# Optimization experiments

Measured on AMD Instinct MI355X. Metric: run time of the kernel, lower is better.

Reference implementation:

```python
import jax, jax.numpy as jnp
import numpy as np

D_IN = 768
D_SAE = 768 * 16  # expansion_factor = 16
K = 64
BATCH = 8192


def setup_inputs() -> dict:
    key = jax.random.key(0)
    k1, k2, k3 = jax.random.split(key, 3)
    x = jax.random.normal(k1, (BATCH, D_IN), dtype=jnp.float32)
    # Kaiming-uniform-ish encoder init (exact init values don't matter for correctness)
    bound = (6.0 / D_IN) ** 0.5
    W_enc = jax.random.uniform(k2, (D_IN, D_SAE), dtype=jnp.float32, minval=-bound, maxval=bound)
    b_enc = jnp.zeros((D_SAE,), dtype=jnp.float32)
    W_dec = jax.random.normal(k3, (D_SAE, D_IN), dtype=jnp.float32) * (1.0 / D_IN ** 0.5)
    # unit-norm decoder rows (per the module's normalize_decoder_weights)
    W_dec = W_dec / (jnp.linalg.norm(W_dec, axis=1, keepdims=True) + 1e-8)
    b_dec = jnp.zeros((D_IN,), dtype=jnp.float32)
    return {"x": x, "W_enc": W_enc, "b_enc": b_enc, "W_dec": W_dec, "b_dec": b_dec}


def reference(x, W_enc, b_enc, W_dec, b_dec):
    # encode: center, dense matmul, ReLU
    pre_acts = jax.nn.relu((x - b_dec) @ W_enc + b_enc)  # [B, d_sae]
    # top-k selection per row, scatter back into dense sparse_acts
    topk_vals, topk_idx = jax.lax.top_k(pre_acts, K)  # [B, K]
    rows = jnp.arange(pre_acts.shape[0])[:, None]  # [B, 1]
    sparse_acts = jnp.zeros_like(pre_acts).at[rows, topk_idx].set(topk_vals)
    # decode: dense matmul + bias
    reconstruction = sparse_acts @ W_dec + b_dec  # [B, d_in]
    return (reconstruction, sparse_acts)
```

## Files before the change

kernel.cpp:

```cpp
#include <hip/hip_runtime.h>
#include <hip/hip_fp16.h>
#include <stdint.h>

#define D_IN   768
#define D_SAE  12288
#define BATCH  8192
#define K_TOP  64
#define CAND_MAX 256

typedef _Float16 f16;
typedef _Float16 v8h __attribute__((ext_vector_type(8)));
typedef float v4f __attribute__((ext_vector_type(4)));

__device__ inline void async16(const void* g, void* l) {
    __builtin_amdgcn_global_load_lds(
        (const __attribute__((address_space(1))) unsigned int*)g,
        (__attribute__((address_space(3))) unsigned int*)l, 16, 0, 0);
}

__global__ __launch_bounds__(256) void k_convert_x(
    const float* __restrict__ x, const float* __restrict__ b_dec,
    f16* __restrict__ xhi, f16* __restrict__ xlo)
{
    int i4 = (blockIdx.x * 256 + threadIdx.x) * 4;
    float4 v = *(const float4*)(x + i4);
    int col = i4 % D_IN;
    float vv[4] = { v.x - b_dec[col], v.y - b_dec[col + 1],
                    v.z - b_dec[col + 2], v.w - b_dec[col + 3] };
    union { short4 s; f16 h[4]; } H, L;
#pragma unroll
    for (int u = 0; u < 4; ++u) {
        H.h[u] = (f16)vv[u];
        L.h[u] = (f16)(vv[u] - (float)H.h[u]);
    }
    *(short4*)(xhi + i4) = H.s;
    *(short4*)(xlo + i4) = L.s;
}

__global__ __launch_bounds__(256) void k_convert_wt(
    const float* __restrict__ W, f16* __restrict__ whiT, f16* __restrict__ wloT)
{
    __shared__ float tile[32][33];
    const int n0 = blockIdx.x * 32;
    const int k0 = blockIdx.y * 32;
    const int c = threadIdx.x & 31;
    const int rr = threadIdx.x >> 5;
#pragma unroll
    for (int s = 0; s < 4; ++s) {
        int r = s * 8 + rr;
        tile[r][c] = W[(size_t)(k0 + r) * D_SAE + n0 + c];
    }
    __syncthreads();
#pragma unroll
    for (int s = 0; s < 4; ++s) {
        int r2 = s * 8 + rr;
        float v = tile[c][r2];
        f16 hi = (f16)v;
        f16 lo = (f16)(v - (float)hi);
        whiT[(size_t)(n0 + r2) * D_IN + k0 + c] = hi;
        wloT[(size_t)(n0 + r2) * D_IN + k0 + c] = lo;
    }
}

__global__ __launch_bounds__(256) void k_gemm_f16(
    const f16* __restrict__ A,
    const f16* __restrict__ Bt,
    const float* __restrict__ b_enc,
    float* __restrict__ out)
{
    __shared__ f16 Asm[128 * 32];
    __shared__ f16 Bsm[128 * 32];
    const int tid  = threadIdx.x;
    const int wave = tid >> 6;
    const int lane = tid & 63;
    const int bn = blockIdx.x * 128;
    const int bm = blockIdx.y * 128;

    const int r16  = lane >> 2;
    const int kc8  = (lane & 3) * 8;
    const int mrow = lane & 15;
    const int quad = lane >> 4;
    const int wm = (wave & 1) * 64;
    const int wn = (wave >> 1) * 64;

    v4f acc[4][4] = {};

    const f16* gA0 = A  + (size_t)(bm + wave * 32 + r16) * D_IN + kc8;
    const f16* gA1 = gA0 + 16 * D_IN;
    const f16* gB0 = Bt + (size_t)(bn + wave * 32 + r16) * D_IN + kc8;
    const f16* gB1 = gB0 + 16 * D_IN;
    f16* lA0 = &Asm[(wave * 32) * 32];
    f16* lA1 = &Asm[(wave * 32 + 16) * 32];
    f16* lB0 = &Bsm[(wave * 32) * 32];
    f16* lB1 = &Bsm[(wave * 32 + 16) * 32];

    for (int k0 = 0; k0 < D_IN; k0 += 32) {
        __syncthreads();
        async16(gA0 + k0, lA0);
        async16(gA1 + k0, lA1);
        async16(gB0 + k0, lB0);
        async16(gB1 + k0, lB1);
        __syncthreads();

        v8h af[4], bf[4];
#pragma unroll
        for (int i = 0; i < 4; ++i)
            af[i] = *(const v8h*)&Asm[(wm + i * 16 + mrow) * 32 + quad * 8];
#pragma unroll
        for (int j = 0; j < 4; ++j)
            bf[j] = *(const v8h*)&Bsm[(wn + j * 16 + mrow) * 32 + quad * 8];

#pragma unroll
        for (int i = 0; i < 4; ++i)
#pragma unroll
            for (int j = 0; j < 4; ++j)
                acc[i][j] = __builtin_amdgcn_mfma_f32_16x16x32_f16(af[i], bf[j], acc[i][j], 0, 0, 0);
    }

#pragma unroll
    for (int i = 0; i < 4; ++i) {
#pragma unroll
        for (int r = 0; r < 4; ++r) {
            int grow = bm + wm + i * 16 + quad * 4 + r;
            float* op = out + (size_t)grow * D_SAE + bn + wn;
#pragma unroll
            for (int j = 0; j < 4; ++j) {
                int c = j * 16 + mrow;
                float val = acc[i][j][r] + b_enc[bn + wn + c];
                op[c] = val > 0.f ? val : 0.f;
            }
        }
    }
}

__global__ __launch_bounds__(256) void k_topk2(
    float* __restrict__ sparse,
    const f16* __restrict__ Xhi, const f16* __restrict__ Xlo,
    const f16* __restrict__ WhiT, const f16* __restrict__ WloT,
    const float* __restrict__ b_enc,
    const float* __restrict__ Wdec,
    const float* __restrict__ b_dec,
    float* __restrict__ recon)
{
    const int row = blockIdx.x;
    const int t = threadIdx.x;
    float* rp = sparse + (size_t)row * D_SAE;

    float v[48];
#pragma unroll
    for (int j = 0; j < 48; ++j) v[j] = rp[j * 256 + t];

    __shared__ unsigned hist[256];
    __shared__ unsigned suf[256];
    __shared__ float sh_cutoff;
    __shared__ int sh_ncand;
    __shared__ int   cand_i[CAND_MAX];
    __shared__ float cand_v[CAND_MAX];
    __shared__ float kept_v[K_TOP];
    __shared__ int   kept_i[K_TOP];
    __shared__ float xr[D_IN];

    const float margin = 0.05f;

    hist[t] = 0;
    if (t == 0) sh_ncand = 0;
    __syncthreads();
#pragma unroll
    for (int j = 0; j < 48; ++j) {
        float x = v[j];
        if (x >= 0.25f) {
            int b = (int)(x * 32.0f); if (b > 255) b = 255;
            atomicAdd(&hist[b], 1u);
        }
    }
    __syncthreads();
    suf[t] = hist[t];
    __syncthreads();
    for (int off = 1; off < 256; off <<= 1) {
        unsigned add = (t + off < 256) ? suf[t + off] : 0u;
        __syncthreads();
        suf[t] += add;
        __syncthreads();
    }
    unsigned total0 = suf[0];
    if (total0 >= K_TOP) {
        if (suf[t] >= K_TOP && (t == 255 || suf[t + 1] < K_TOP))
            sh_cutoff = fmaxf((float)t * (1.0f / 32.0f) - margin, 1e-30f);
    } else {
        __syncthreads();
        hist[t] = 0;
        __syncthreads();
#pragma unroll
        for (int j = 0; j < 48; ++j) {
            float x = v[j];
            if (x > 0.0f && x < 0.25f) {
                int b = (int)(x * 1024.0f); if (b > 255) b = 255;
                atomicAdd(&hist[b], 1u);
            }
        }
        __syncthreads();
        suf[t] = hist[t];
        __syncthreads();
        for (int off = 1; off < 256; off <<= 1) {
            unsigned add = (t + off < 256) ? suf[t + off] : 0u;
            __syncthreads();
            suf[t] += add;
            __syncthreads();
        }
        unsigned need = K_TOP - total0;
        if (suf[0] >= need) {
            if (suf[t] >= need && (t == 255 || suf[t + 1] < need))
                sh_cutoff = fmaxf((float)t * (1.0f / 1024.0f) - margin, 1e-30f);
        } else {
            if (t == 0) sh_cutoff = 1e-30f;
        }
    }
    __syncthreads();
    const float cutoff = sh_cutoff;

#pragma unroll
    for (int j = 0; j < 48; ++j) {
        float x = v[j];
        if (x >= cutoff) {
            int pos = atomicAdd(&sh_ncand, 1);
            if (pos < CAND_MAX) { cand_i[pos] = j * 256 + t; cand_v[pos] = x; }
        }
    }
    __syncthreads();
    int ncand = sh_ncand; if (ncand > CAND_MAX) ncand = CAND_MAX;

    for (int k = t; k < D_IN; k += 256)
        xr[k] = (float)Xhi[(size_t)row * D_IN + k] + (float)Xlo[(size_t)row * D_IN + k];
    __syncthreads();
    for (int c = t; c < ncand; c += 256) {
        const f16* wh = WhiT + (size_t)cand_i[c] * D_IN;
        const f16* wl = WloT + (size_t)cand_i[c] * D_IN;
        float acc = 0.f;
        for (int k = 0; k < D_IN; k += 8) {
            v8h hv = *(const v8h*)(wh + k);
            v8h lv = *(const v8h*)(wl + k);
#pragma unroll
            for (int u = 0; u < 8; ++u)
                acc += xr[k + u] * ((float)hv[u] + (float)lv[u]);
        }
        acc += b_enc[cand_i[c]];
        cand_v[c] = acc > 0.f ? acc : 0.f;
    }
    __syncthreads();

    for (int c = t; c < ncand; c += 256) {
        float vc = cand_v[c]; int ic = cand_i[c];
        int r = 0;
        for (int m = 0; m < ncand; ++m) {
            float vm = cand_v[m];
            r += (vm > vc || (vm == vc && cand_i[m] < ic)) ? 1 : 0;
        }
        if (r < K_TOP) { kept_v[r] = vc; kept_i[r] = ic; }
    }
    __syncthreads();
    int nk = ncand < K_TOP ? ncand : K_TOP;

#pragma unroll
    for (int j = 0; j < 12; ++j) {
        float4 z = {0.f, 0.f, 0.f, 0.f};
        *(float4*)(rp + ((size_t)j * 256 + t) * 4) = z;
    }
    __syncthreads();
    if (t < nk) rp[kept_i[t]] = kept_v[t];

    float r0 = b_dec[t], r1 = b_dec[t + 256], r2 = b_dec[t + 512];
    for (int m = 0; m < nk; ++m) {
        float val = kept_v[m];
        const float* wr = Wdec + (size_t)kept_i[m] * D_IN;
        r0 += val * wr[t];
        r1 += val * wr[t + 256];
        r2 += val * wr[t + 512];
    }
    float* rc = recon + (size_t)row * D_IN;
    rc[t] = r0; rc[t + 256] = r1; rc[t + 512] = r2;
}

extern "C" void kernel_launch(void* const* d_in, const int* in_sizes, int n_in,
                              void* d_out, int out_size, void* d_ws, size_t ws_size,
                              hipStream_t stream) {
    const float* x     = (const float*)d_in[0];
    const float* W_enc = (const float*)d_in[1];
    const float* b_enc = (const float*)d_in[2];
    const float* W_dec = (const float*)d_in[3];
    const float* b_dec = (const float*)d_in[4];
    float* out    = (float*)d_out;
    float* recon  = out;
    float* sparse = out + (size_t)BATCH * D_IN;

    const size_t xplane = (size_t)BATCH * D_IN;
    const size_t wplane = (size_t)D_SAE * D_IN;
    f16* xhi  = (f16*)d_ws;
    f16* xlo  = xhi + xplane;
    f16* whiT = xlo + xplane;
    f16* wloT = whiT + wplane;

    k_convert_x<<<xplane / 1024, 256, 0, stream>>>(x, b_dec, xhi, xlo);
    k_convert_wt<<<dim3(D_SAE / 32, D_IN / 32), 256, 0, stream>>>(W_enc, whiT, wloT);
    k_gemm_f16<<<dim3(D_SAE / 128, BATCH / 128), 256, 0, stream>>>(xhi, whiT, b_enc, sparse);
    k_topk2<<<BATCH, 256, 0, stream>>>(sparse, xhi, xlo, whiT, wloT, b_enc, W_dec, b_dec, recon);
}
```

Before: 1.358 ms.

## Store approximate pre-activations as fp16 and double the GEMM K step

The approximate encoder GEMM now writes ReLU pre-activations as fp16 into the first half of each sparse output row, using nontemporal stores, instead of fp32. The top-k kernel reads them back with vector loads and rebuilds candidate indices to match. This halves the traffic of the dense intermediate written and read between the two kernels. The GEMM also loads two 32-wide K slices per barrier pair, and the zero-fill and reconstruction writes use nontemporal stores. The lower fp16 precision only affects candidate screening, since candidates are recomputed exactly and a margin is applied.

Measured after the change: 1.240 ms. -8.7%, faster.

```diff
diff --git a/kernel.cpp b/kernel.cpp
--- a/kernel.cpp
+++ b/kernel.cpp
@@ -66,10 +66,10 @@
     const f16* __restrict__ A,
     const f16* __restrict__ Bt,
     const float* __restrict__ b_enc,
-    float* __restrict__ out)
+    f16* __restrict__ outap)
 {
-    __shared__ f16 Asm[128 * 32];
-    __shared__ f16 Bsm[128 * 32];
+    __shared__ f16 Asm[2][128 * 32];
+    __shared__ f16 Bsm[2][128 * 32];
     const int tid  = threadIdx.x;
     const int wave = tid >> 6;
     const int lane = tid & 63;
@@ -85,36 +85,44 @@
 
     v4f acc[4][4] = {};
 
-    const f16* gA0 = A  + (size_t)(bm + wave * 32 + r16) * D_IN + kc8;
-    const f16* gA1 = gA0 + 16 * D_IN;
-    const f16* gB0 = Bt + (size_t)(bn + wave * 32 + r16) * D_IN + kc8;
-    const f16* gB1 = gB0 + 16 * D_IN;
-    f16* lA0 = &Asm[(wave * 32) * 32];
-    f16* lA1 = &Asm[(wave * 32 + 16) * 32];
-    f16* lB0 = &Bsm[(wave * 32) * 32];
-    f16* lB1 = &Bsm[(wave * 32 + 16) * 32];
-
-    for (int k0 = 0; k0 < D_IN; k0 += 32) {
-        __syncthreads();
-        async16(gA0 + k0, lA0);
-        async16(gA1 + k0, lA1);
-        async16(gB0 + k0, lB0);
-        async16(gB1 + k0, lB1);
-        __syncthreads();
-
-        v8h af[4], bf[4];
-#pragma unroll
-        for (int i = 0; i < 4; ++i)
-            af[i] = *(const v8h*)&Asm[(wm + i * 16 + mrow) * 32 + quad * 8];
-#pragma unroll
-        for (int j = 0; j < 4; ++j)
-            bf[j] = *(const v8h*)&Bsm[(wn + j * 16 + mrow) * 32 + quad * 8];
-
-#pragma unroll
-        for (int i = 0; i < 4; ++i)
+    const f16* gA = A  + (size_t)(bm + wave * 32 + r16) * D_IN + kc8;
+    const f16* gB = Bt + (size_t)(bn + wave * 32 + r16) * D_IN + kc8;
+    f16* lA0  = &Asm[0][(wave * 32) * 32];
+    f16* lA0b = &Asm[0][(wave * 32 + 16) * 32];
+    f16* lB0  = &Bsm[0][(wave * 32) * 32];
+    f16* lB0b = &Bsm[0][(wave * 32 + 16) * 32];
+    f16* lA1  = &Asm[1][(wave * 32) * 32];
+    f16* lA1b = &Asm[1][(wave * 32 + 16) * 32];
+    f16* lB1  = &Bsm[1][(wave * 32) * 32];
+    f16* lB1b = &Bsm[1][(wave * 32 + 16) * 32];
+
+    for (int k0 = 0; k0 < D_IN; k0 += 64) {
+        __syncthreads();
+        async16(gA + k0,               lA0);
+        async16(gA + k0 + 16 * D_IN,   lA0b);
+        async16(gB + k0,               lB0);
+        async16(gB + k0 + 16 * D_IN,   lB0b);
+        async16(gA + k0 + 32,              lA1);
+        async16(gA + k0 + 32 + 16 * D_IN,  lA1b);
+        async16(gB + k0 + 32,              lB1);
+        async16(gB + k0 + 32 + 16 * D_IN,  lB1b);
+        __syncthreads();
+
+#pragma unroll
+        for (int s = 0; s < 2; ++s) {
+            v8h af[4], bf[4];
+#pragma unroll
+            for (int i = 0; i < 4; ++i)
+                af[i] = *(const v8h*)&Asm[s][(wm + i * 16 + mrow) * 32 + quad * 8];
 #pragma unroll
             for (int j = 0; j < 4; ++j)
-                acc[i][j] = __builtin_amdgcn_mfma_f32_16x16x32_f16(af[i], bf[j], acc[i][j], 0, 0, 0);
+                bf[j] = *(const v8h*)&Bsm[s][(wn + j * 16 + mrow) * 32 + quad * 8];
+#pragma unroll
+            for (int i = 0; i < 4; ++i)
+#pragma unroll
+                for (int j = 0; j < 4; ++j)
+                    acc[i][j] = __builtin_amdgcn_mfma_f32_16x16x32_f16(af[i], bf[j], acc[i][j], 0, 0, 0);
+        }
     }
 
 #pragma unroll
@@ -122,12 +130,12 @@
 #pragma unroll
         for (int r = 0; r < 4; ++r) {
             int grow = bm + wm + i * 16 + quad * 4 + r;
-            float* op = out + (size_t)grow * D_SAE + bn + wn;
+            f16* op = outap + (size_t)grow * (2 * D_SAE) + bn + wn;
 #pragma unroll
             for (int j = 0; j < 4; ++j) {
                 int c = j * 16 + mrow;
                 float val = acc[i][j][r] + b_enc[bn + wn + c];
-                op[c] = val > 0.f ? val : 0.f;
+                __builtin_nontemporal_store((f16)(val > 0.f ? val : 0.f), op + c);
             }
         }
     }
@@ -145,10 +153,12 @@
     const int row = blockIdx.x;
     const int t = threadIdx.x;
     float* rp = sparse + (size_t)row * D_SAE;
-
-    float v[48];
-#pragma unroll
-    for (int j = 0; j < 48; ++j) v[j] = rp[j * 256 + t];
+    const f16* ap = (const f16*)rp;
+
+    v8h av[6];
+#pragma unroll
+    for (int j = 0; j < 6; ++j)
+        av[j] = __builtin_nontemporal_load((const v8h*)(ap + ((size_t)j * 256 + t) * 8));
 
     __shared__ unsigned hist[256];
     __shared__ unsigned suf[256];
@@ -166,13 +176,15 @@
     if (t == 0) sh_ncand = 0;
     __syncthreads();
 #pragma unroll
-    for (int j = 0; j < 48; ++j) {
-        float x = v[j];
-        if (x >= 0.25f) {
-            int b = (int)(x * 32.0f); if (b > 255) b = 255;
-            atomicAdd(&hist[b], 1u);
-        }
-    }
+    for (int j = 0; j < 6; ++j)
+#pragma unroll
+        for (int u = 0; u < 8; ++u) {
+            float x = (float)av[j][u];
+            if (x >= 0.25f) {
+                int b = (int)(x * 32.0f); if (b > 255) b = 255;
+                atomicAdd(&hist[b], 1u);
+            }
+        }
     __syncthreads();
     suf[t] = hist[t];
     __syncthreads();
@@ -191,13 +203,15 @@
         hist[t] = 0;
         __syncthreads();
 #pragma unroll
-        for (int j = 0; j < 48; ++j) {
-            float x = v[j];
-            if (x > 0.0f && x < 0.25f) {
-                int b = (int)(x * 1024.0f); if (b > 255) b = 255;
-                atomicAdd(&hist[b], 1u);
+        for (int j = 0; j < 6; ++j)
+#pragma unroll
+            for (int u = 0; u < 8; ++u) {
+                float x = (float)av[j][u];
+                if (x > 0.0f && x < 0.25f) {
+                    int b = (int)(x * 1024.0f); if (b > 255) b = 255;
+                    atomicAdd(&hist[b], 1u);
+                }
             }
-        }
         __syncthreads();
         suf[t] = hist[t];
         __syncthreads();
@@ -219,13 +233,15 @@
     const float cutoff = sh_cutoff;
 
 #pragma unroll
-    for (int j = 0; j < 48; ++j) {
-        float x = v[j];
-        if (x >= cutoff) {
-            int pos = atomicAdd(&sh_ncand, 1);
-            if (pos < CAND_MAX) { cand_i[pos] = j * 256 + t; cand_v[pos] = x; }
-        }
-    }
+    for (int j = 0; j < 6; ++j)
+#pragma unroll
+        for (int u = 0; u < 8; ++u) {
+            float x = (float)av[j][u];
+            if (x >= cutoff) {
+                int pos = atomicAdd(&sh_ncand, 1);
+                if (pos < CAND_MAX) { cand_i[pos] = (j * 256 + t) * 8 + u; cand_v[pos] = x; }
+            }
+        }
     __syncthreads();
     int ncand = sh_ncand; if (ncand > CAND_MAX) ncand = CAND_MAX;
 
@@ -262,8 +278,8 @@
 
 #pragma unroll
     for (int j = 0; j < 12; ++j) {
-        float4 z = {0.f, 0.f, 0.f, 0.f};
-        *(float4*)(rp + ((size_t)j * 256 + t) * 4) = z;
+        v4f z = {0.f, 0.f, 0.f, 0.f};
+        __builtin_nontemporal_store(z, (v4f*)(rp + ((size_t)j * 256 + t) * 4));
     }
     __syncthreads();
     if (t < nk) rp[kept_i[t]] = kept_v[t];
@@ -277,7 +293,9 @@
         r2 += val * wr[t + 512];
     }
     float* rc = recon + (size_t)row * D_IN;
-    rc[t] = r0; rc[t + 256] = r1; rc[t + 512] = r2;
+    __builtin_nontemporal_store(r0, rc + t);
+    __builtin_nontemporal_store(r1, rc + t + 256);
+    __builtin_nontemporal_store(r2, rc + t + 512);
 }
 
 extern "C" void kernel_launch(void* const* d_in, const int* in_sizes, int n_in,
@@ -301,6 +319,6 @@
 
     k_convert_x<<<xplane / 1024, 256, 0, stream>>>(x, b_dec, xhi, xlo);
     k_convert_wt<<<dim3(D_SAE / 32, D_IN / 32), 256, 0, stream>>>(W_enc, whiT, wloT);
-    k_gemm_f16<<<dim3(D_SAE / 128, BATCH / 128), 256, 0, stream>>>(xhi, whiT, b_enc, sparse);
+    k_gemm_f16<<<dim3(D_SAE / 128, BATCH / 128), 256, 0, stream>>>(xhi, whiT, b_enc, (f16*)sparse);
     k_topk2<<<BATCH, 256, 0, stream>>>(sparse, xhi, xlo, whiT, wloT, b_enc, W_dec, b_dec, recon);
 }
```
